# Kernel tuning notes

Hardware: AMD Instinct MI355X
Metric: run time of the kernel (lower is better)

The kernel has to match this reference:

```python
import jax, jax.numpy as jnp
import numpy as np

B, H, L, D = 4, 16, 1024, 64
DROP_P = 0.5


def setup_inputs() -> dict:
    key = jax.random.key(0)
    kq, kk, kv, kg, kd = jax.random.split(key, 5)
    q = jax.random.normal(kq, (B, H, L, D), dtype=jnp.float32)
    k = jax.random.normal(kk, (B, H, L, D), dtype=jnp.float32)
    v = jax.random.normal(kv, (B, H, L, D), dtype=jnp.float32)
    # standard Gumbel(0,1) noise consumed by gumbel_softmax
    gumbel_noise = jax.random.gumbel(kg, (B, H, L, L), dtype=jnp.float32)
    # inverted-dropout mask: keep w.p. (1-p), scale kept by 1/(1-p)
    keep = jax.random.bernoulli(kd, 1.0 - DROP_P, (B, H, L, L))
    drop_mask = keep.astype(jnp.float32) / (1.0 - DROP_P)
    return {"q": q, "k": k, "v": v, "gumbel_noise": gumbel_noise, "drop_mask": drop_mask}


def reference(q, k, v, gumbel_noise, drop_mask):
    q = jax.nn.elu(q)
    k = jax.nn.elu(k)
    v = jax.nn.elu(v)
    scale = q.shape[-1] ** -0.5  # qk / sqrt(d)
    qk = jnp.einsum("bhld,bhmd->bhlm", q, k) * scale
    # gumbel_softmax(hard=True), tau=1
    logits = qk + gumbel_noise
    y_soft = jax.nn.softmax(logits, axis=-1)
    y_hard = jax.nn.one_hot(jnp.argmax(y_soft, axis=-1), logits.shape[-1], dtype=y_soft.dtype)
    y = jax.lax.stop_gradient(y_hard - y_soft) + y_soft  # straight-through
    dropped = y * drop_mask  # dropout p=0.5
    out = jnp.einsum("bhlm,bhmd->bhld", dropped, v)
    return out
```

## Files before the change

### kernel.cpp

```cpp
#include <hip/hip_runtime.h>
#include <math.h>


#define BH      64
#define SEQ     1024
#define DIM     64
#define NSPLIT  4
#define MR      (SEQ / NSPLIT)
#define NTILES  (MR / 32)
#define NTHR    256

typedef short bf16x8 __attribute__((ext_vector_type(8)));
typedef float f32x16 __attribute__((ext_vector_type(16)));

__device__ __forceinline__ float eluf(float x) { return x > 0.0f ? x : expm1f(x); }

__device__ __forceinline__ unsigned f2bf_bits(float x) {
    unsigned u = __float_as_uint(x);
    return (u + 0x7fffu + ((u >> 16) & 1u)) >> 16;
}

__device__ __forceinline__ void split_bf16(float x, short& h, short& l) {
    unsigned hb = f2bf_bits(x);
    float hf = __uint_as_float(hb << 16);
    h = (short)hb;
    l = (short)f2bf_bits(x - hf);
}

__device__ __forceinline__ void top2_update(float v, int m,
                                            float& b1, int& i1,
                                            float& b2, int& i2) {
    bool gt1 = v > b1;
    bool gt2 = v > b2;
    float nb2 = gt1 ? b1 : (gt2 ? v : b2);
    int   ni2 = gt1 ? i1 : (gt2 ? m : i2);
    b1 = gt1 ? v : b1;
    i1 = gt1 ? m : i1;
    b2 = nb2; i2 = ni2;
}

__global__ __launch_bounds__(NTHR)
void prep_k_kernel(const float4* __restrict__ k4,
                   short4* __restrict__ khi, short4* __restrict__ klo) {
    int f = blockIdx.x * NTHR + threadIdx.x;
    float4 val = k4[f];
    short4 hv, lv;
    split_bf16(eluf(val.x), hv.x, lv.x);
    split_bf16(eluf(val.y), hv.y, lv.y);
    split_bf16(eluf(val.z), hv.z, lv.z);
    split_bf16(eluf(val.w), hv.w, lv.w);
    khi[f] = hv;
    klo[f] = lv;
}

__global__ __launch_bounds__(NTHR, 3)
void score_top2_kernel(const float* __restrict__ q,
                       const short* __restrict__ khi,
                       const short* __restrict__ klo,
                       const float* __restrict__ gum,
                       int4* __restrict__ top2out) {
    const int w    = threadIdx.x >> 6;
    const int lane = threadIdx.x & 63;
    const int lrow = lane & 31;
    const int half = lane >> 5;

    const int x     = blockIdx.x & 7;
    const int j     = blockIdx.x >> 3;
    const int bh    = x * 8 + (j & 7);
    const int ltile = j >> 3;
    const int l0    = ltile * 32;
    const int ms    = w * MR;

    const size_t row = (size_t)bh * SEQ + l0 + lrow;

    bf16x8 qh[4], ql[4];
    {
        const float4* q4 = (const float4*)q + row * 16;
        #pragma unroll
        for (int ks = 0; ks < 4; ++ks) {
            float4 a = q4[ks * 4 + half * 2];
            float4 b = q4[ks * 4 + half * 2 + 1];
            float e[8] = { eluf(a.x), eluf(a.y), eluf(a.z), eluf(a.w),
                           eluf(b.x), eluf(b.y), eluf(b.z), eluf(b.w) };
            #pragma unroll
            for (int t = 0; t < 8; ++t) {
                short h, l;
                split_bf16(e[t], h, l);
                qh[ks][t] = h;
                ql[ks][t] = l;
            }
        }
    }

    const short* kh_base = khi + ((size_t)(bh * SEQ + ms + lrow) * 64 + half * 8);
    const short* kl_base = klo + ((size_t)(bh * SEQ + ms + lrow) * 64 + half * 8);
    const float* gp      = gum + (row << 10) + ms + half * 4;

    float b1 = -INFINITY, b2 = -INFINITY;
    int   i1 = 0, i2 = 0;

    bf16x8 ah[2][4], al[2][4];
    float  g[2][16];

    #pragma unroll
    for (int ks = 0; ks < 4; ++ks) {
        ah[0][ks] = *(const bf16x8*)(kh_base + ks * 16);
        al[0][ks] = *(const bf16x8*)(kl_base + ks * 16);
    }
    #pragma unroll
    for (int qd = 0; qd < 4; ++qd) {
        float4 t4 = *(const float4*)(gp + qd * 8);
        g[0][qd * 4 + 0] = t4.x; g[0][qd * 4 + 1] = t4.y;
        g[0][qd * 4 + 2] = t4.z; g[0][qd * 4 + 3] = t4.w;
    }

    #pragma unroll
    for (int t = 0; t < NTILES; ++t) {
        const int cur = t & 1, nxt = cur ^ 1;
        if (t < NTILES - 1) {
            #pragma unroll
            for (int ks = 0; ks < 4; ++ks) {
                ah[nxt][ks] = *(const bf16x8*)(kh_base + (t + 1) * 2048 + ks * 16);
                al[nxt][ks] = *(const bf16x8*)(kl_base + (t + 1) * 2048 + ks * 16);
            }
            #pragma unroll
            for (int qd = 0; qd < 4; ++qd) {
                float4 t4 = *(const float4*)(gp + (t + 1) * 32 + qd * 8);
                g[nxt][qd * 4 + 0] = t4.x; g[nxt][qd * 4 + 1] = t4.y;
                g[nxt][qd * 4 + 2] = t4.z; g[nxt][qd * 4 + 3] = t4.w;
            }
        }

        f32x16 acc = (f32x16)0.0f;
        #pragma unroll
        for (int ks = 0; ks < 4; ++ks) {
            acc = __builtin_amdgcn_mfma_f32_32x32x16_bf16(ah[cur][ks], qh[ks], acc, 0, 0, 0);
            acc = __builtin_amdgcn_mfma_f32_32x32x16_bf16(ah[cur][ks], ql[ks], acc, 0, 0, 0);
            acc = __builtin_amdgcn_mfma_f32_32x32x16_bf16(al[cur][ks], qh[ks], acc, 0, 0, 0);
        }

        const int mb = ms + t * 32 + half * 4;
        #pragma unroll
        for (int r = 0; r < 16; ++r) {
            float lg = fmaf(acc[r], 0.125f, g[cur][r]);
            top2_update(lg, mb + (r & 3) + 8 * (r >> 2), b1, i1, b2, i2);
        }
    }

    {
        float ob1 = __shfl_xor(b1, 32);
        int   oi1 = __shfl_xor(i1, 32);
        float ob2 = __shfl_xor(b2, 32);
        int   oi2 = __shfl_xor(i2, 32);
        top2_update(ob1, oi1, b1, i1, b2, i2);
        top2_update(ob2, oi2, b1, i1, b2, i2);
    }
    if (half == 0) {
        top2out[row * NSPLIT + w] = make_int4(__float_as_int(b1), i1,
                                              __float_as_int(b2), i2);
    }
}

__global__ __launch_bounds__(NTHR)
void fixup_out_kernel(const float* __restrict__ q,
                      const float* __restrict__ k,
                      const float* __restrict__ v,
                      const float* __restrict__ gum,
                      const float* __restrict__ drop,
                      const int4* __restrict__ top2in,
                      float* __restrict__ out) {
    __shared__ int   msf[128];
    __shared__ float dropv[128];

    const int rloc = threadIdx.x >> 1;
    const int cand = threadIdx.x & 1;
    const size_t row = (size_t)blockIdx.x * 128 + rloc;
    const int bh = (int)(row >> 10);

    float b1 = -INFINITY, b2 = -INFINITY;
    int   i1 = 0, i2 = 0;
    #pragma unroll
    for (int s = 0; s < NSPLIT; ++s) {
        int4 p = top2in[row * NSPLIT + s];
        top2_update(__int_as_float(p.x), p.y, b1, i1, b2, i2);
        top2_update(__int_as_float(p.z), p.w, b1, i1, b2, i2);
    }
    const int m = cand ? i2 : i1;

    const float4* q4r = (const float4*)q + row * 16;
    const float4* k4r = (const float4*)k + ((size_t)bh * SEQ + m) * 16;
    double s = 0.0;
    #pragma unroll
    for (int i = 0; i < 16; ++i) {
        float4 a = q4r[i], b = k4r[i];
        s += (double)eluf(a.x) * (double)eluf(b.x);
        s += (double)eluf(a.y) * (double)eluf(b.y);
        s += (double)eluf(a.z) * (double)eluf(b.z);
        s += (double)eluf(a.w) * (double)eluf(b.w);
    }
    double L  = s * 0.125 + (double)gum[(row << 10) + m];
    double Lo = __shfl_xor(L, 1);
    int    mo = __shfl_xor(m, 1);
    const int mstar = (L > Lo || (L == Lo && m < mo)) ? m : mo;
    if (cand == 0) {
        msf[rloc]   = mstar;
        dropv[rloc] = drop[(row << 10) + mstar];
    }
    __syncthreads();

    const int bh0 = (int)(((size_t)blockIdx.x * 128) >> 10);
    const float4* v4 = (const float4*)v + (size_t)bh0 * SEQ * 16;
    float4* o4 = (float4*)out + (size_t)blockIdx.x * 128 * 16;
    #pragma unroll
    for (int i = 0; i < 8; ++i) {
        int f  = threadIdx.x + NTHR * i;
        int rr = f >> 4, qd = f & 15;
        int   mm = msf[rr];
        float dm = dropv[rr];
        float4 vv = v4[mm * 16 + qd];
        float4 ov;
        ov.x = dm * eluf(vv.x); ov.y = dm * eluf(vv.y);
        ov.z = dm * eluf(vv.z); ov.w = dm * eluf(vv.w);
        o4[rr * 16 + qd] = ov;
    }
}

extern "C" void kernel_launch(void* const* d_in, const int* in_sizes, int n_in,
                              void* d_out, int out_size, void* d_ws, size_t ws_size,
                              hipStream_t stream) {
    const float* q    = (const float*)d_in[0];
    const float* k    = (const float*)d_in[1];
    const float* v    = (const float*)d_in[2];
    const float* gum  = (const float*)d_in[3];
    const float* drop = (const float*)d_in[4];
    float* out = (float*)d_out;

    short* khi = (short*)d_ws;
    short* klo = khi + (size_t)BH * SEQ * DIM;
    int4*  top2 = (int4*)((char*)d_ws + (size_t)2 * BH * SEQ * DIM * sizeof(short));

    prep_k_kernel<<<dim3((BH * SEQ * DIM / 4) / NTHR), dim3(NTHR), 0, stream>>>(
        (const float4*)k, (short4*)khi, (short4*)klo);
    score_top2_kernel<<<dim3(BH * (SEQ / 32) * NSPLIT / 4), dim3(NTHR), 0, stream>>>(
        q, khi, klo, gum, top2);
    fixup_out_kernel<<<dim3((BH * SEQ) / 128), dim3(NTHR), 0, stream>>>(
        q, k, v, gum, drop, top2, out);
}
```

Before: 574.9 us.

## Fuse top-2 fixup and output gather into the score kernel

Merges the separate fixup/output kernel into the score kernel. Per-wave top-2 partials now go through shared memory instead of a global workspace, and after a block barrier the same block refines the winner in fp64 and writes its 32 output rows. This removes one kernel launch and the global round trip of the top-2 buffer. In exchange it adds a serialized tail where only 64 threads do the fixup, plus extra shared memory that could affect occupancy.

```diff
diff --git a/kernel.cpp b/kernel.cpp
--- a/kernel.cpp
+++ b/kernel.cpp
@@ -54,11 +54,18 @@
 }
 
 __global__ __launch_bounds__(NTHR, 3)
-void score_top2_kernel(const float* __restrict__ q,
-                       const short* __restrict__ khi,
-                       const short* __restrict__ klo,
-                       const float* __restrict__ gum,
-                       int4* __restrict__ top2out) {
+void score_fused_kernel(const float* __restrict__ q,
+                        const short* __restrict__ khi,
+                        const short* __restrict__ klo,
+                        const float* __restrict__ gum,
+                        const float* __restrict__ k,
+                        const float* __restrict__ v,
+                        const float* __restrict__ drop,
+                        float* __restrict__ out) {
+    __shared__ int4  part[32][NSPLIT + 1];
+    __shared__ int   msf[32];
+    __shared__ float dropv[32];
+
     const int w    = threadIdx.x >> 6;
     const int lane = threadIdx.x & 63;
     const int lrow = lane & 31;
@@ -156,64 +163,54 @@
         top2_update(ob2, oi2, b1, i1, b2, i2);
     }
     if (half == 0) {
-        top2out[row * NSPLIT + w] = make_int4(__float_as_int(b1), i1,
-                                              __float_as_int(b2), i2);
-    }
-}
-
-__global__ __launch_bounds__(NTHR)
-void fixup_out_kernel(const float* __restrict__ q,
-                      const float* __restrict__ k,
-                      const float* __restrict__ v,
-                      const float* __restrict__ gum,
-                      const float* __restrict__ drop,
-                      const int4* __restrict__ top2in,
-                      float* __restrict__ out) {
-    __shared__ int   msf[128];
-    __shared__ float dropv[128];
-
-    const int rloc = threadIdx.x >> 1;
-    const int cand = threadIdx.x & 1;
-    const size_t row = (size_t)blockIdx.x * 128 + rloc;
-    const int bh = (int)(row >> 10);
-
-    float b1 = -INFINITY, b2 = -INFINITY;
-    int   i1 = 0, i2 = 0;
-    #pragma unroll
-    for (int s = 0; s < NSPLIT; ++s) {
-        int4 p = top2in[row * NSPLIT + s];
-        top2_update(__int_as_float(p.x), p.y, b1, i1, b2, i2);
-        top2_update(__int_as_float(p.z), p.w, b1, i1, b2, i2);
-    }
-    const int m = cand ? i2 : i1;
-
-    const float4* q4r = (const float4*)q + row * 16;
-    const float4* k4r = (const float4*)k + ((size_t)bh * SEQ + m) * 16;
-    double s = 0.0;
-    #pragma unroll
-    for (int i = 0; i < 16; ++i) {
-        float4 a = q4r[i], b = k4r[i];
-        s += (double)eluf(a.x) * (double)eluf(b.x);
-        s += (double)eluf(a.y) * (double)eluf(b.y);
-        s += (double)eluf(a.z) * (double)eluf(b.z);
-        s += (double)eluf(a.w) * (double)eluf(b.w);
-    }
-    double L  = s * 0.125 + (double)gum[(row << 10) + m];
-    double Lo = __shfl_xor(L, 1);
-    int    mo = __shfl_xor(m, 1);
-    const int mstar = (L > Lo || (L == Lo && m < mo)) ? m : mo;
-    if (cand == 0) {
-        msf[rloc]   = mstar;
-        dropv[rloc] = drop[(row << 10) + mstar];
+        part[lrow][w] = make_int4(__float_as_int(b1), i1,
+                                  __float_as_int(b2), i2);
     }
     __syncthreads();
 
-    const int bh0 = (int)(((size_t)blockIdx.x * 128) >> 10);
-    const float4* v4 = (const float4*)v + (size_t)bh0 * SEQ * 16;
-    float4* o4 = (float4*)out + (size_t)blockIdx.x * 128 * 16;
-    #pragma unroll
-    for (int i = 0; i < 8; ++i) {
-        int f  = threadIdx.x + NTHR * i;
+    const int tid = threadIdx.x;
+    if (tid < 64) {
+        const int rloc = tid >> 1;
+        const int cand = tid & 1;
+        const size_t rrow = (size_t)bh * SEQ + l0 + rloc;
+
+        float fb1 = -INFINITY, fb2 = -INFINITY;
+        int   fi1 = 0, fi2 = 0;
+        #pragma unroll
+        for (int s = 0; s < NSPLIT; ++s) {
+            int4 p = part[rloc][s];
+            top2_update(__int_as_float(p.x), p.y, fb1, fi1, fb2, fi2);
+            top2_update(__int_as_float(p.z), p.w, fb1, fi1, fb2, fi2);
+        }
+        const int m = cand ? fi2 : fi1;
+
+        const float4* q4r = (const float4*)q + rrow * 16;
+        const float4* k4r = (const float4*)k + ((size_t)bh * SEQ + m) * 16;
+        double s = 0.0;
+        #pragma unroll
+        for (int i = 0; i < 16; ++i) {
+            float4 a = q4r[i], b = k4r[i];
+            s += (double)eluf(a.x) * (double)eluf(b.x);
+            s += (double)eluf(a.y) * (double)eluf(b.y);
+            s += (double)eluf(a.z) * (double)eluf(b.z);
+            s += (double)eluf(a.w) * (double)eluf(b.w);
+        }
+        double L  = s * 0.125 + (double)gum[(rrow << 10) + m];
+        double Lo = __shfl_xor(L, 1);
+        int    mo = __shfl_xor(m, 1);
+        const int mstar = (L > Lo || (L == Lo && m < mo)) ? m : mo;
+        if (cand == 0) {
+            msf[rloc]   = mstar;
+            dropv[rloc] = drop[(rrow << 10) + mstar];
+        }
+    }
+    __syncthreads();
+
+    const float4* v4 = (const float4*)v + (size_t)bh * SEQ * 16;
+    float4* o4 = (float4*)out + ((size_t)bh * SEQ + l0) * 16;
+    #pragma unroll
+    for (int i = 0; i < 2; ++i) {
+        int f  = tid + NTHR * i;
         int rr = f >> 4, qd = f & 15;
         int   mm = msf[rr];
         float dm = dropv[rr];
@@ -237,12 +234,9 @@
 
     short* khi = (short*)d_ws;
     short* klo = khi + (size_t)BH * SEQ * DIM;
-    int4*  top2 = (int4*)((char*)d_ws + (size_t)2 * BH * SEQ * DIM * sizeof(short));
 
     prep_k_kernel<<<dim3((BH * SEQ * DIM / 4) / NTHR), dim3(NTHR), 0, stream>>>(
         (const float4*)k, (short4*)khi, (short4*)klo);
-    score_top2_kernel<<<dim3(BH * (SEQ / 32) * NSPLIT / 4), dim3(NTHR), 0, stream>>>(
-        q, khi, klo, gum, top2);
-    fixup_out_kernel<<<dim3((BH * SEQ) / 128), dim3(NTHR), 0, stream>>>(
-        q, k, v, gum, drop, top2, out);
-}
+    score_fused_kernel<<<dim3(BH * (SEQ / 32) * NSPLIT / 4), dim3(NTHR), 0, stream>>>(
+        q, khi, klo, gum, k, v, drop, out);
+}
```

Result: slower. 586.7 us (+2.1%).

## Drop bf16 lo-split of K, pool 16 candidates, exact fixup within delta

Applied to the files above, without the earlier changes.

Removes the low bf16 half of K, so the score pass issues two MFMAs per k-step instead of three and reads half the K workspace. The 1/8 scale is folded into K, and the accumulator is seeded with the Gumbel noise. Each row now keeps 16 top-2 candidates, one set per half-wave and split. The fixup kernel recomputes fp64 logits only for candidates within a fixed margin of the max, and skips that work when only one candidate is close. This relies on the bf16 error staying below the margin, which holds statistically but is not guaranteed, so it risks a wrong argmax on near ties. The fixup grid is also reshaped to 16 rows per block.

```diff
diff --git a/kernel.cpp b/kernel.cpp
--- a/kernel.cpp
+++ b/kernel.cpp
@@ -9,6 +9,9 @@
 #define MR      (SEQ / NSPLIT)
 #define NTILES  (MR / 32)
 #define NTHR    256
+#define NPOOL   8
+#define DELTA   0.05f
+#define FIXROWS 16
 
 typedef short bf16x8 __attribute__((ext_vector_type(8)));
 typedef float f32x16 __attribute__((ext_vector_type(16)));
@@ -40,25 +43,22 @@
 }
 
 __global__ __launch_bounds__(NTHR)
-void prep_k_kernel(const float4* __restrict__ k4,
-                   short4* __restrict__ khi, short4* __restrict__ klo) {
+void prep_k_kernel(const float4* __restrict__ k4, short4* __restrict__ khi) {
     int f = blockIdx.x * NTHR + threadIdx.x;
     float4 val = k4[f];
-    short4 hv, lv;
-    split_bf16(eluf(val.x), hv.x, lv.x);
-    split_bf16(eluf(val.y), hv.y, lv.y);
-    split_bf16(eluf(val.z), hv.z, lv.z);
-    split_bf16(eluf(val.w), hv.w, lv.w);
+    short4 hv;
+    hv.x = (short)f2bf_bits(0.125f * eluf(val.x));
+    hv.y = (short)f2bf_bits(0.125f * eluf(val.y));
+    hv.z = (short)f2bf_bits(0.125f * eluf(val.z));
+    hv.w = (short)f2bf_bits(0.125f * eluf(val.w));
     khi[f] = hv;
-    klo[f] = lv;
-}
-
-__global__ __launch_bounds__(NTHR, 3)
-void score_top2_kernel(const float* __restrict__ q,
-                       const short* __restrict__ khi,
-                       const short* __restrict__ klo,
-                       const float* __restrict__ gum,
-                       int4* __restrict__ top2out) {
+}
+
+__global__ __launch_bounds__(NTHR, 4)
+void score_kernel(const float* __restrict__ q,
+                  const short* __restrict__ khi,
+                  const float* __restrict__ gum,
+                  int4* __restrict__ pool) {
     const int w    = threadIdx.x >> 6;
     const int lane = threadIdx.x & 63;
     const int lrow = lane & 31;
@@ -93,72 +93,49 @@
     }
 
     const short* kh_base = khi + ((size_t)(bh * SEQ + ms + lrow) * 64 + half * 8);
-    const short* kl_base = klo + ((size_t)(bh * SEQ + ms + lrow) * 64 + half * 8);
     const float* gp      = gum + (row << 10) + ms + half * 4;
 
     float b1 = -INFINITY, b2 = -INFINITY;
     int   i1 = 0, i2 = 0;
 
-    bf16x8 ah[2][4], al[2][4];
-    float  g[2][16];
-
-    #pragma unroll
-    for (int ks = 0; ks < 4; ++ks) {
+    bf16x8 ah[2][4];
+    union GU { f32x16 v; float4 f4[4]; };
+    GU g[2];
+
+    #pragma unroll
+    for (int ks = 0; ks < 4; ++ks)
         ah[0][ks] = *(const bf16x8*)(kh_base + ks * 16);
-        al[0][ks] = *(const bf16x8*)(kl_base + ks * 16);
-    }
-    #pragma unroll
-    for (int qd = 0; qd < 4; ++qd) {
-        float4 t4 = *(const float4*)(gp + qd * 8);
-        g[0][qd * 4 + 0] = t4.x; g[0][qd * 4 + 1] = t4.y;
-        g[0][qd * 4 + 2] = t4.z; g[0][qd * 4 + 3] = t4.w;
-    }
+    #pragma unroll
+    for (int qd = 0; qd < 4; ++qd)
+        g[0].f4[qd] = *(const float4*)(gp + qd * 8);
 
     #pragma unroll
     for (int t = 0; t < NTILES; ++t) {
         const int cur = t & 1, nxt = cur ^ 1;
         if (t < NTILES - 1) {
             #pragma unroll
-            for (int ks = 0; ks < 4; ++ks) {
+            for (int ks = 0; ks < 4; ++ks)
                 ah[nxt][ks] = *(const bf16x8*)(kh_base + (t + 1) * 2048 + ks * 16);
-                al[nxt][ks] = *(const bf16x8*)(kl_base + (t + 1) * 2048 + ks * 16);
-            }
             #pragma unroll
-            for (int qd = 0; qd < 4; ++qd) {
-                float4 t4 = *(const float4*)(gp + (t + 1) * 32 + qd * 8);
-                g[nxt][qd * 4 + 0] = t4.x; g[nxt][qd * 4 + 1] = t4.y;
-                g[nxt][qd * 4 + 2] = t4.z; g[nxt][qd * 4 + 3] = t4.w;
-            }
-        }
-
-        f32x16 acc = (f32x16)0.0f;
+            for (int qd = 0; qd < 4; ++qd)
+                g[nxt].f4[qd] = *(const float4*)(gp + (t + 1) * 32 + qd * 8);
+        }
+
+        f32x16 acc = g[cur].v;
         #pragma unroll
         for (int ks = 0; ks < 4; ++ks) {
             acc = __builtin_amdgcn_mfma_f32_32x32x16_bf16(ah[cur][ks], qh[ks], acc, 0, 0, 0);
             acc = __builtin_amdgcn_mfma_f32_32x32x16_bf16(ah[cur][ks], ql[ks], acc, 0, 0, 0);
-            acc = __builtin_amdgcn_mfma_f32_32x32x16_bf16(al[cur][ks], qh[ks], acc, 0, 0, 0);
         }
 
         const int mb = ms + t * 32 + half * 4;
         #pragma unroll
-        for (int r = 0; r < 16; ++r) {
-            float lg = fmaf(acc[r], 0.125f, g[cur][r]);
-            top2_update(lg, mb + (r & 3) + 8 * (r >> 2), b1, i1, b2, i2);
-        }
-    }
-
-    {
-        float ob1 = __shfl_xor(b1, 32);
-        int   oi1 = __shfl_xor(i1, 32);
-        float ob2 = __shfl_xor(b2, 32);
-        int   oi2 = __shfl_xor(i2, 32);
-        top2_update(ob1, oi1, b1, i1, b2, i2);
-        top2_update(ob2, oi2, b1, i1, b2, i2);
-    }
-    if (half == 0) {
-        top2out[row * NSPLIT + w] = make_int4(__float_as_int(b1), i1,
-                                              __float_as_int(b2), i2);
-    }
+        for (int r = 0; r < 16; ++r)
+            top2_update(acc[r], mb + (r & 3) + 8 * (r >> 2), b1, i1, b2, i2);
+    }
+
+    pool[row * NPOOL + w + NSPLIT * half] =
+        make_int4(__float_as_int(b1), i1, __float_as_int(b2), i2);
 }
 
 __global__ __launch_bounds__(NTHR)
@@ -167,62 +144,74 @@
                       const float* __restrict__ v,
                       const float* __restrict__ gum,
                       const float* __restrict__ drop,
-                      const int4* __restrict__ top2in,
+                      const int4* __restrict__ pool,
                       float* __restrict__ out) {
-    __shared__ int   msf[128];
-    __shared__ float dropv[128];
-
-    const int rloc = threadIdx.x >> 1;
-    const int cand = threadIdx.x & 1;
-    const size_t row = (size_t)blockIdx.x * 128 + rloc;
+    __shared__ int   msf[FIXROWS];
+    __shared__ float dropv[FIXROWS];
+
+    const int tid  = threadIdx.x;
+    const int rloc = tid >> 4;
+    const int cand = tid & 15;
+    const size_t row = (size_t)blockIdx.x * FIXROWS + rloc;
     const int bh = (int)(row >> 10);
 
-    float b1 = -INFINITY, b2 = -INFINITY;
-    int   i1 = 0, i2 = 0;
-    #pragma unroll
-    for (int s = 0; s < NSPLIT; ++s) {
-        int4 p = top2in[row * NSPLIT + s];
-        top2_update(__int_as_float(p.x), p.y, b1, i1, b2, i2);
-        top2_update(__int_as_float(p.z), p.w, b1, i1, b2, i2);
-    }
-    const int m = cand ? i2 : i1;
-
-    const float4* q4r = (const float4*)q + row * 16;
-    const float4* k4r = (const float4*)k + ((size_t)bh * SEQ + m) * 16;
-    double s = 0.0;
-    #pragma unroll
-    for (int i = 0; i < 16; ++i) {
-        float4 a = q4r[i], b = k4r[i];
-        s += (double)eluf(a.x) * (double)eluf(b.x);
-        s += (double)eluf(a.y) * (double)eluf(b.y);
-        s += (double)eluf(a.z) * (double)eluf(b.z);
-        s += (double)eluf(a.w) * (double)eluf(b.w);
-    }
-    double L  = s * 0.125 + (double)gum[(row << 10) + m];
-    double Lo = __shfl_xor(L, 1);
-    int    mo = __shfl_xor(m, 1);
-    const int mstar = (L > Lo || (L == Lo && m < mo)) ? m : mo;
+    int4 p = pool[row * NPOOL + (cand >> 1)];
+    float val = (cand & 1) ? __int_as_float(p.z) : __int_as_float(p.x);
+    int   m   = (cand & 1) ? p.w : p.y;
+
+    float mx = val;
+    #pragma unroll
+    for (int s = 1; s < 16; s <<= 1) mx = fmaxf(mx, __shfl_xor(mx, s));
+
+    const bool active = (val >= mx - DELTA);
+    unsigned long long bal = __ballot(active);
+    const int gsh  = ((tid & 63) >> 4) << 4;
+    const int acnt = __popcll((bal >> gsh) & 0xFFFFull);
+
+    double Lv;
+    if (!active) {
+        Lv = -1.0e300;
+    } else if (acnt <= 1) {
+        Lv = 1.0;
+    } else {
+        const float4* q4r = (const float4*)q + row * 16;
+        const float4* k4r = (const float4*)k + ((size_t)bh * SEQ + m) * 16;
+        double s = 0.0;
+        #pragma unroll
+        for (int i = 0; i < 16; ++i) {
+            float4 a = q4r[i], b = k4r[i];
+            s += (double)eluf(a.x) * (double)eluf(b.x);
+            s += (double)eluf(a.y) * (double)eluf(b.y);
+            s += (double)eluf(a.z) * (double)eluf(b.z);
+            s += (double)eluf(a.w) * (double)eluf(b.w);
+        }
+        Lv = s * 0.125 + (double)gum[(row << 10) + m];
+    }
+
+    int mm = m;
+    #pragma unroll
+    for (int s = 1; s < 16; s <<= 1) {
+        double Lo = __shfl_xor(Lv, s);
+        int    mo = __shfl_xor(mm, s);
+        if (Lo > Lv || (Lo == Lv && mo < mm)) { Lv = Lo; mm = mo; }
+    }
     if (cand == 0) {
-        msf[rloc]   = mstar;
-        dropv[rloc] = drop[(row << 10) + mstar];
+        msf[rloc]   = mm;
+        dropv[rloc] = drop[(row << 10) + mm];
     }
     __syncthreads();
 
-    const int bh0 = (int)(((size_t)blockIdx.x * 128) >> 10);
+    const int bh0 = (int)(((size_t)blockIdx.x * FIXROWS) >> 10);
     const float4* v4 = (const float4*)v + (size_t)bh0 * SEQ * 16;
-    float4* o4 = (float4*)out + (size_t)blockIdx.x * 128 * 16;
-    #pragma unroll
-    for (int i = 0; i < 8; ++i) {
-        int f  = threadIdx.x + NTHR * i;
-        int rr = f >> 4, qd = f & 15;
-        int   mm = msf[rr];
-        float dm = dropv[rr];
-        float4 vv = v4[mm * 16 + qd];
-        float4 ov;
-        ov.x = dm * eluf(vv.x); ov.y = dm * eluf(vv.y);
-        ov.z = dm * eluf(vv.z); ov.w = dm * eluf(vv.w);
-        o4[rr * 16 + qd] = ov;
-    }
+    float4* o4 = (float4*)out + (size_t)blockIdx.x * FIXROWS * 16;
+    const int rr = tid >> 4, qd = tid & 15;
+    const int   mmv = msf[rr];
+    const float dm  = dropv[rr];
+    float4 vv = v4[mmv * 16 + qd];
+    float4 ov;
+    ov.x = dm * eluf(vv.x); ov.y = dm * eluf(vv.y);
+    ov.z = dm * eluf(vv.z); ov.w = dm * eluf(vv.w);
+    o4[rr * 16 + qd] = ov;
 }
 
 extern "C" void kernel_launch(void* const* d_in, const int* in_sizes, int n_in,
@@ -235,14 +224,13 @@
     const float* drop = (const float*)d_in[4];
     float* out = (float*)d_out;
 
-    short* khi = (short*)d_ws;
-    short* klo = khi + (size_t)BH * SEQ * DIM;
-    int4*  top2 = (int4*)((char*)d_ws + (size_t)2 * BH * SEQ * DIM * sizeof(short));
+    short* khi  = (short*)d_ws;
+    int4*  pool = (int4*)((char*)d_ws + (size_t)BH * SEQ * DIM * sizeof(short));
 
     prep_k_kernel<<<dim3((BH * SEQ * DIM / 4) / NTHR), dim3(NTHR), 0, stream>>>(
-        (const float4*)k, (short4*)khi, (short4*)klo);
-    score_top2_kernel<<<dim3(BH * (SEQ / 32) * NSPLIT / 4), dim3(NTHR), 0, stream>>>(
-        q, khi, klo, gum, top2);
-    fixup_out_kernel<<<dim3((BH * SEQ) / 128), dim3(NTHR), 0, stream>>>(
-        q, k, v, gum, drop, top2, out);
-}
+        (const float4*)k, (short4*)khi);
+    score_kernel<<<dim3(BH * (SEQ / 32) * NSPLIT / 4), dim3(NTHR), 0, stream>>>(
+        q, khi, gum, pool);
+    fixup_out_kernel<<<dim3((BH * SEQ) / FIXROWS), dim3(NTHR), 0, stream>>>(
+        q, k, v, gum, drop, pool, out);
+}
```

After: 573.7 us. About the same (-0.2%).
